# Kernel tuning notes

Hardware: AMD Instinct MI355X
Metric: run time of the kernel (lower is better)

Reference implementation:

```python
import jax, jax.numpy as jnp
import numpy as np

CONF_THRES = 0.7
IOU_THRES = 0.45
TOP_K = 1000  # max candidates kept per image after confidence filtering (YOLOv5 max_nms-style cap)
IMG_SIZE = 640.0


def _box_iou(boxes):
    """Pairwise IoU of [K,4] xyxy boxes -> [K,K]."""
    area = (boxes[:, 2] - boxes[:, 0]) * (boxes[:, 3] - boxes[:, 1])
    lt = jnp.maximum(boxes[:, None, :2], boxes[None, :, :2])
    rb = jnp.minimum(boxes[:, None, 2:], boxes[None, :, 2:])
    wh = jnp.clip(rb - lt, 0.0)
    inter = wh[..., 0] * wh[..., 1]
    return inter / (area[:, None] + area[None, :] - inter + 1e-7)


def _nms_single(pred):
    """YOLOv5-style NMS for one image. pred: [N, 9] = xywh, obj, cls_conf, pitch, yaw, roll.
    Returns fixed-shape padded detections [TOP_K, 9] and keep mask [TOP_K]."""
    obj = pred[:, 4]
    conf = obj * pred[:, 5]  # nc=1: conf = obj_conf * cls_conf
    valid = (obj > CONF_THRES) & (conf > CONF_THRES)
    score = jnp.where(valid, conf, -1.0)

    top_scores, idx = jax.lax.top_k(score, TOP_K)
    p = pred[idx]  # [TOP_K, 9]
    xy, wh = p[:, :2], p[:, 2:4]
    boxes = jnp.concatenate([xy - wh * 0.5, xy + wh * 0.5], axis=-1)  # xywh -> xyxy

    keep0 = top_scores > CONF_THRES
    iou = _box_iou(boxes)  # [TOP_K, TOP_K]
    ar = jnp.arange(TOP_K)

    # Greedy NMS: boxes are score-sorted; box j is suppressed if a kept earlier box overlaps > thresh.
    def body(i, keep):
        sup = (iou[i] > IOU_THRES) & (ar > i) & keep[i]
        return keep & (~sup)

    keep = jax.lax.fori_loop(0, TOP_K, body, keep0)

    cls = jnp.zeros((TOP_K, 1), boxes.dtype)  # single class (head)
    out = jnp.concatenate([boxes, top_scores[:, None], cls, p[:, 6:9]], axis=-1)  # [TOP_K, 9]
    out = out * keep[:, None].astype(out.dtype)  # zero padded/suppressed rows
    return out, keep


def setup_inputs() -> dict:
    key = jax.random.key(0)
    B, N = 32, 25200
    r = jax.random.uniform(key, (B, N, 9), dtype=jnp.float32)
    xy = r[..., :2] * IMG_SIZE                 # box centers in pixels
    wh = r[..., 2:4] * 128.0 + 4.0             # box sizes 4..132 px
    obj = r[..., 4:5]                          # objectness in [0,1)
    cls = r[..., 5:6] * 0.5 + 0.5              # class conf in [0.5,1)
    ang = (r[..., 6:9] - 0.5) * 2.0            # normalized pitch/yaw/roll
    prediction = jnp.concatenate([xy, wh, obj, cls, ang], axis=-1)
    return {"prediction": prediction}


def reference(prediction):
    out, keep = jax.vmap(_nms_single)(prediction)
    return out, keep
```

## Files before the change

kernel.cpp:

```cpp
#include <hip/hip_runtime.h>
#include <stdint.h>

#pragma clang fp contract(off)

#define BATCH 32
#define NPRED 25200
#define ROWF 9
#define TOPK 1000
#define SUBS 8
#define ROWS_PER_SUB (NPRED / SUBS)
#define SUBCAP 512
#define CONF_T 0.7f
#define IOU_T 0.45f
#define KW 16
#define SUPROW 1024
#define TKROW 1024

typedef unsigned long long u64;
typedef unsigned int u32;

#define WS_CAND 0
#define WS_BX   (1048576)
#define WS_SA   (WS_BX + 524288)
#define WS_SUP  (WS_SA + 524288)


__device__ __forceinline__ u64 readlane64(u64 v, int l) {
    u32 lo = __builtin_amdgcn_readlane((u32)v, (u32)l);
    u32 hi = __builtin_amdgcn_readlane((u32)(v >> 32), (u32)l);
    return ((u64)hi << 32) | lo;
}

__global__ __launch_bounds__(512) void compact_sort_kernel(const float* __restrict__ pred,
                                                           u64* __restrict__ cand_ws,
                                                           float4* __restrict__ bx_ws,
                                                           float4* __restrict__ sa_ws) {
    __shared__ u64 skey[SUBCAP];
    __shared__ u32 cnt;
    int bs = blockIdx.x;
    int b = bs >> 3, s = bs & 7;
    int tid = threadIdx.x;
    if (tid == 0) cnt = 0;
    skey[tid] = 0;
    if (tid < 128) {
        float4 z = make_float4(0.f, 0.f, 0.f, 0.f);
        bx_ws[(size_t)b * TKROW + s * 128 + tid] = z;
        sa_ws[(size_t)b * TKROW + s * 128 + tid] = z;
    }
    __syncthreads();

    int r0 = s * ROWS_PER_SUB;
    const int NCH = (ROWS_PER_SUB + 511) / 512;
    float objv[NCH], clsv[NCH];
#pragma unroll
    for (int k = 0; k < NCH; ++k) {
        int r = tid + k * 512;
        if (r < ROWS_PER_SUB) {
            size_t base = ((size_t)b * NPRED + r0 + r) * ROWF;
            objv[k] = pred[base + 4];
            clsv[k] = pred[base + 5];
        }
    }
#pragma unroll
    for (int k = 0; k < NCH; ++k) {
        int r = tid + k * 512;
        if (r < ROWS_PER_SUB) {
            float conf = objv[k] * clsv[k];
            if (objv[k] > CONF_T && conf > CONF_T) {
                int row = r0 + r;
                u32 slot = atomicAdd(&cnt, 1u);
                if (slot < SUBCAP)
                    skey[slot] = ((u64)__float_as_uint(conf) << 32) | (u64)(u32)(~(u32)row);
            }
        }
    }
    __syncthreads();
    for (int k = 2; k <= SUBCAP; k <<= 1) {
        for (int j = k >> 1; j > 0; j >>= 1) {
            int t = tid, p = t ^ j;
            if (p > t) {
                u64 a = skey[t], c2 = skey[p];
                bool desc = ((t & k) == 0);
                if (desc ? (a < c2) : (a > c2)) { skey[t] = c2; skey[p] = a; }
            }
            __syncthreads();
        }
    }
    cand_ws[(size_t)bs * SUBCAP + tid] = skey[tid];
}

__global__ __launch_bounds__(512) void rank_kernel(const float* __restrict__ pred,
                                                   const u64* __restrict__ cand_ws,
                                                   float4* __restrict__ bx_ws,
                                                   float4* __restrict__ sa_ws) {
    __shared__ u64 lists[SUBS * SUBCAP];
    int bs = blockIdx.x;
    int b = bs >> 3, s = bs & 7;
    int tid = threadIdx.x;
    const u64* src = cand_ws + (size_t)b * SUBS * SUBCAP;
    for (int t = tid; t < SUBS * SUBCAP; t += 512) lists[t] = src[t];
    __syncthreads();
    u64 key = lists[(s << 9) + tid];
    if (key) {
        int lo[SUBS];
#pragma unroll
        for (int l = 0; l < SUBS; ++l) lo[l] = 0;
#pragma unroll
        for (int w2 = SUBCAP; w2 >= 1; w2 >>= 1) {
#pragma unroll
            for (int l = 0; l < SUBS; ++l) {
                int p = lo[l] + w2;
                if (p <= SUBCAP && lists[(l << 9) + p - 1] > key) lo[l] = p;
            }
        }
        int rank = 0;
#pragma unroll
        for (int l = 0; l < SUBS; ++l) rank += lo[l];
        if (rank < TOPK) {
            u32 r = ~(u32)key;
            const float* p = pred + ((size_t)b * NPRED + r) * ROWF;
            float x = p[0], y = p[1], wd = p[2], hh = p[3];
            float4 box = make_float4(x - wd * 0.5f, y - hh * 0.5f,
                                     x + wd * 0.5f, y + hh * 0.5f);
            float4 sa = make_float4(__uint_as_float((u32)(key >> 32)),
                                    p[6], p[7], p[8]);
            bx_ws[(size_t)b * TKROW + rank] = box;
            sa_ws[(size_t)b * TKROW + rank] = sa;
        }
    }
}

__global__ __launch_bounds__(1024) void supmat_kernel(const float4* __restrict__ bx_ws,
                                                      u64* __restrict__ sup_g) {
    __shared__ float4 bx_s[1024];
    __shared__ float  ar_s[1024];
    int b = blockIdx.x >> 3, q = blockIdx.x & 7;
    int tid = threadIdx.x;
    {
        float4 box = bx_ws[(size_t)b * TKROW + tid];
        bx_s[tid] = box;
        ar_s[tid] = (box.z - box.x) * (box.w - box.y);
    }
    __syncthreads();
    int wave = tid >> 6, lane = tid & 63;
    for (int pass = 0; pass < 2; ++pass) {
        int t = (pass == 0) ? (q * 16 + wave) : ((wave == 15) ? 128 + q : 136);
        if (t >= 136) continue;
        int iw = 0, rem = t, c = 16;
        while (rem >= c) { rem -= c; c--; iw++; }
        int jw = iw + rem;
        int i = iw * 64 + lane;
        bool act = i < TOPK;
        float4 bi = act ? bx_s[i] : make_float4(0.f, 0.f, 0.f, 0.f);
        float ai = act ? ar_s[i] : 0.f;
        u64 m = 0;
        int jbase = jw << 6;
        int jend = jbase + 64; if (jend > TOPK) jend = TOPK;
        for (int j = jbase; j < jend; ++j) {
            float4 bj = bx_s[j];
            float aj = ar_s[j];
            float lx = fmaxf(bi.x, bj.x);
            float ly = fmaxf(bi.y, bj.y);
            float rx = fminf(bi.z, bj.z);
            float ry = fminf(bi.w, bj.w);
            float iw2 = rx - lx; iw2 = iw2 > 0.f ? iw2 : 0.f;
            float ih = ry - ly; ih = ih > 0.f ? ih : 0.f;
            float inter = iw2 * ih;
            float den = ai + aj - inter + 1e-7f;
            float iou = inter / den;
            if (act && j > i && iou > IOU_T) m |= 1ull << (j - jbase);
        }
        if (act) sup_g[((size_t)b * KW + jw) * SUPROW + i] = m;
    }
}

__global__ __launch_bounds__(1024) void scan_out_kernel(const float4* __restrict__ bx_ws,
                                                        const float4* __restrict__ sa_ws,
                                                        const u64* __restrict__ sup_g,
                                                        float* __restrict__ out,
                                                        float* __restrict__ keepout) {
    __shared__ u64 keep_lds[KW];
    __shared__ u64 acc_lds;
    int b = blockIdx.x, tid = threadIdx.x;
    int w = tid >> 6, lane = tid & 63;
    const u64* S = sup_g + (size_t)b * KW * SUPROW;

    float4 sa = sa_ws[(size_t)b * TKROW + tid];
    u64 keep0 = __ballot(sa.x != 0.f);
    if (lane == 0) keep_lds[w] = keep0;

    u64 sup_reg[KW];
    u64 diagreg = 0;
#pragma unroll
    for (int bi = 0; bi < KW; ++bi) {
        sup_reg[bi] = S[(size_t)w * SUPROW + (bi << 6) + lane];
        if (bi == w) diagreg = sup_reg[bi];
    }
    __syncthreads();

    u64 nzmask = __ballot(diagreg != 0);

#pragma unroll
    for (int bi = 0; bi < KW; ++bi) {
        if (w == bi) {
            u64 cur = keep_lds[bi];
            u64 active = cur & nzmask;
            while (active) {
                int i = __ffsll((long long)active) - 1;
                u64 wi = readlane64(diagreg, i);
                active &= active - 1;
                cur &= ~wi;
                active &= ~wi;
            }
            if (lane == 0) { keep_lds[bi] = cur; acc_lds = cur; }
        }
        __syncthreads();
        if (w > bi) {
            u64 A = acc_lds;
            u64 myv = sup_reg[bi];
            bool accb = (A >> lane) & 1ull;
            u64 lanes = __ballot(accb && myv != 0ull);
            if (lanes) {
                u64 wred = 0;
                while (lanes) {
                    int l = __ffsll((long long)lanes) - 1;
                    wred |= readlane64(myv, l);
                    lanes &= lanes - 1;
                }
                if (lane == 0) keep_lds[w] &= ~wred;
            }
        }
        __syncthreads();
    }

    if (tid < TOPK) {
        bool kp = ((keep_lds[w] >> lane) & 1ull) != 0;
        float4 bx = bx_ws[(size_t)b * TKROW + tid];
        size_t ob = ((size_t)b * TOPK + tid) * ROWF;
        out[ob + 0] = kp ? bx.x : 0.f;
        out[ob + 1] = kp ? bx.y : 0.f;
        out[ob + 2] = kp ? bx.z : 0.f;
        out[ob + 3] = kp ? bx.w : 0.f;
        out[ob + 4] = kp ? sa.x : 0.f;
        out[ob + 5] = 0.f;
        out[ob + 6] = kp ? sa.y : 0.f;
        out[ob + 7] = kp ? sa.z : 0.f;
        out[ob + 8] = kp ? sa.w : 0.f;
        keepout[(size_t)b * TOPK + tid] = kp ? 1.0f : 0.0f;
    }
}

extern "C" void kernel_launch(void* const* d_in, const int* in_sizes, int n_in,
                              void* d_out, int out_size, void* d_ws, size_t ws_size,
                              hipStream_t stream) {
    const float* pred = (const float*)d_in[0];
    float* out = (float*)d_out;
    float* keepout = out + (size_t)BATCH * TOPK * ROWF;
    char* ws = (char*)d_ws;
    u64* cand_ws = (u64*)(ws + WS_CAND);
    float4* bx_ws = (float4*)(ws + WS_BX);
    float4* sa_ws = (float4*)(ws + WS_SA);
    u64* sup_g = (u64*)(ws + WS_SUP);

    compact_sort_kernel<<<BATCH * SUBS, 512, 0, stream>>>(pred, cand_ws, bx_ws, sa_ws);
    rank_kernel<<<BATCH * SUBS, 512, 0, stream>>>(pred, cand_ws, bx_ws, sa_ws);
    supmat_kernel<<<BATCH * SUBS, 1024, 0, stream>>>(bx_ws, sup_g);
    scan_out_kernel<<<BATCH, 1024, 0, stream>>>(bx_ws, sa_ws, sup_g, out, keepout);
}
```

Measured before the change: 124.5 us.

## Use wave shuffles in bitonic sort, readlane broadcasts in IoU, skip unused loads

The bitonic sort now keeps each key in a register. Compare-exchange steps with stride under 64 use cross-lane xor shuffles, and only larger strides go through LDS with barriers, which removes most __syncthreads. The IoU mask kernel loads the 64 j-boxes once per lane and broadcasts them with readlane instead of reading LDS every iteration. The scan kernel skips loading suppression blocks above the diagonal. Risks are extra readlane instructions and the index bounds on bx_s reads that are no longer guarded.

```diff
diff --git a/kernel.cpp b/kernel.cpp
--- a/kernel.cpp
+++ b/kernel.cpp
@@ -28,6 +28,14 @@
 __device__ __forceinline__ u64 readlane64(u64 v, int l) {
     u32 lo = __builtin_amdgcn_readlane((u32)v, (u32)l);
     u32 hi = __builtin_amdgcn_readlane((u32)(v >> 32), (u32)l);
+    return ((u64)hi << 32) | lo;
+}
+__device__ __forceinline__ float readlanef(float v, int l) {
+    return __uint_as_float(__builtin_amdgcn_readlane(__float_as_uint(v), (u32)l));
+}
+__device__ __forceinline__ u64 shflxor64(u64 v, int m) {
+    u32 lo = __shfl_xor((u32)v, m, 64);
+    u32 hi = __shfl_xor((u32)(v >> 32), m, 64);
     return ((u64)hi << 32) | lo;
 }
 
@@ -75,18 +83,30 @@
         }
     }
     __syncthreads();
+
+    u64 key = skey[tid];
+    bool wrote = true;
     for (int k = 2; k <= SUBCAP; k <<= 1) {
         for (int j = k >> 1; j > 0; j >>= 1) {
-            int t = tid, p = t ^ j;
-            if (p > t) {
-                u64 a = skey[t], c2 = skey[p];
-                bool desc = ((t & k) == 0);
-                if (desc ? (a < c2) : (a > c2)) { skey[t] = c2; skey[p] = a; }
-            }
-            __syncthreads();
-        }
-    }
-    cand_ws[(size_t)bs * SUBCAP + tid] = skey[tid];
+            bool desc = ((tid & k) == 0);
+            bool up = ((tid & j) == 0);
+            u64 part;
+            if (j >= 64) {
+                if (!wrote) { __syncthreads(); skey[tid] = key; }
+                __syncthreads();
+                part = skey[tid ^ j];
+                wrote = false;
+            } else {
+                part = shflxor64(key, j);
+                wrote = false;
+            }
+            bool takemax = (desc == up);
+            u64 mx = key > part ? key : part;
+            u64 mn = key > part ? part : key;
+            key = takemax ? mx : mn;
+        }
+    }
+    cand_ws[(size_t)bs * SUBCAP + tid] = key;
 }
 
 __global__ __launch_bounds__(512) void rank_kernel(const float* __restrict__ pred,
@@ -151,24 +171,28 @@
         int jw = iw + rem;
         int i = iw * 64 + lane;
         bool act = i < TOPK;
-        float4 bi = act ? bx_s[i] : make_float4(0.f, 0.f, 0.f, 0.f);
-        float ai = act ? ar_s[i] : 0.f;
+        float4 bi4 = bx_s[i];
+        float ai = ar_s[i];
+        float4 bja = bx_s[(jw << 6) + lane];
+        float aja = ar_s[(jw << 6) + lane];
         u64 m = 0;
         int jbase = jw << 6;
-        int jend = jbase + 64; if (jend > TOPK) jend = TOPK;
-        for (int j = jbase; j < jend; ++j) {
-            float4 bj = bx_s[j];
-            float aj = ar_s[j];
-            float lx = fmaxf(bi.x, bj.x);
-            float ly = fmaxf(bi.y, bj.y);
-            float rx = fminf(bi.z, bj.z);
-            float ry = fminf(bi.w, bj.w);
+        for (int l2 = 0; l2 < 64; ++l2) {
+            float bjx = readlanef(bja.x, l2);
+            float bjy = readlanef(bja.y, l2);
+            float bjz = readlanef(bja.z, l2);
+            float bjw = readlanef(bja.w, l2);
+            float aj  = readlanef(aja, l2);
+            float lx = fmaxf(bi4.x, bjx);
+            float ly = fmaxf(bi4.y, bjy);
+            float rx = fminf(bi4.z, bjz);
+            float ry = fminf(bi4.w, bjw);
             float iw2 = rx - lx; iw2 = iw2 > 0.f ? iw2 : 0.f;
             float ih = ry - ly; ih = ih > 0.f ? ih : 0.f;
             float inter = iw2 * ih;
             float den = ai + aj - inter + 1e-7f;
             float iou = inter / den;
-            if (act && j > i && iou > IOU_T) m |= 1ull << (j - jbase);
+            if (act && (jbase + l2) > i && iou > IOU_T) m |= 1ull << l2;
         }
         if (act) sup_g[((size_t)b * KW + jw) * SUPROW + i] = m;
     }
@@ -193,7 +217,9 @@
     u64 diagreg = 0;
 #pragma unroll
     for (int bi = 0; bi < KW; ++bi) {
-        sup_reg[bi] = S[(size_t)w * SUPROW + (bi << 6) + lane];
+        sup_reg[bi] = 0;
+        if (bi <= w)
+            sup_reg[bi] = S[(size_t)w * SUPROW + (bi << 6) + lane];
         if (bi == w) diagreg = sup_reg[bi];
     }
     __syncthreads();
```

New measurement: 123.6 us (median of 2 runs). No clear change (-0.8%).
